# Performance work log

Measured on AMD Instinct MI355X. Metric: run time of the kernel, lower is better.

## Reference

```python
import jax, jax.numpy as jnp
import numpy as np

V, F, D, C = 100000, 512, 512, 128      # graph nodes, raw feat dim, internal_dim, num_classes
N1, S1, B1 = 36864, 32768, 4096         # layer-1 dstsrc / src / dst counts
S2, B2 = 3584, 512                      # layer-2 src / dst counts


def setup_inputs() -> dict:
    key = jax.random.key(0)
    ks = jax.random.split(key, 11)
    features = jax.random.normal(ks[0], (V, F), jnp.float32)
    src_nodes = jax.random.randint(ks[1], (N1,), 0, V)
    dst_idx1 = jax.random.randint(ks[2], (B1,), 0, N1)
    src_idx1 = jax.random.randint(ks[3], (S1,), 0, N1)
    # row-normalized diffusion matrix (minibatch generator produces mean-normalized adjacency)
    dif_mat1 = jax.random.uniform(ks[4], (B1, S1), jnp.float32) / S1
    dst_idx2 = jax.random.randint(ks[5], (B2,), 0, B1)
    src_idx2 = jax.random.randint(ks[6], (S2,), 0, B1)
    dif_mat2 = jax.random.uniform(ks[7], (B2, S2), jnp.float32) / S2
    # Glorot-ish weight init
    w1 = jax.random.normal(ks[8], (2 * F, D), jnp.float32) / np.float32(np.sqrt(2 * F))
    w2 = jax.random.normal(ks[9], (2 * D, D), jnp.float32) / np.float32(np.sqrt(2 * D))
    w_cls = jax.random.normal(ks[10], (D, C), jnp.float32) / np.float32(np.sqrt(D))
    return dict(features=features, src_nodes=src_nodes,
                dst_idx1=dst_idx1, src_idx1=src_idx1, dif_mat1=dif_mat1,
                dst_idx2=dst_idx2, src_idx2=src_idx2, dif_mat2=dif_mat2,
                w1=w1, w2=w2, w_cls=w_cls)


def _mean_aggregate(x, dst_idx, src_idx, dif_mat, w):
    # boolean_mask -> gather at selected indices
    agg = dif_mat @ x[src_idx]                       # [B, F_in]
    cat = jnp.concatenate([agg, x[dst_idx]], axis=1)  # [B, 2*F_in]
    return jax.nn.relu(cat @ w)                       # [B, D]


def reference(features, src_nodes, dst_idx1, src_idx1, dif_mat1,
              dst_idx2, src_idx2, dif_mat2, w1, w2, w_cls):
    x = features[src_nodes]                           # RawFeature: gather [N1, F]
    x = _mean_aggregate(x, dst_idx1, src_idx1, dif_mat1, w1)   # [B1, D]
    x = _mean_aggregate(x, dst_idx2, src_idx2, dif_mat2, w2)   # [B2, D]
    return jax.nn.softmax(x @ w_cls, axis=-1)          # classifier [B2, C]
```

## Files before the change

### kernel.cpp

```cpp
#include <hip/hip_runtime.h>

typedef unsigned short u16;
typedef unsigned int u32;
typedef __attribute__((ext_vector_type(8))) short short8;
typedef __attribute__((ext_vector_type(4))) float f32x4;
typedef __attribute__((ext_vector_type(8))) u16 ushort8v;

__device__ __forceinline__ u16 f2bf(float f) {
    union { float f; u32 u; } v; v.f = f;
    return (u16)((v.u + 0x7FFFu + ((v.u >> 16) & 1u)) >> 16);
}
__device__ __forceinline__ u32 pack2bf(float a, float b) {
    union { float f; u32 u; } x, y; x.f = a; y.f = b;
    u32 ra = x.u + 0x7FFFu + ((x.u >> 16) & 1u);
    u32 rb = y.u + 0x7FFFu + ((y.u >> 16) & 1u);
    return (ra >> 16) | (rb & 0xFFFF0000u);
}

__global__ __launch_bounds__(256) void gather_transpose_bf16(
    const float* __restrict__ src, const int* __restrict__ lvl1,
    const int* __restrict__ lvl2, u16* __restrict__ outT, int S)
{
    __shared__ u16 tile[32][514];
    const int s0 = blockIdx.x * 32;
    const int tid = threadIdx.x;
    const int r = tid >> 3;
    const int fb = (tid & 7) * 4;

    int row = lvl1[s0 + r];
    if (lvl2) row = lvl2[row];
    const float* sp = src + (size_t)row * 512;
    #pragma unroll
    for (int j = 0; j < 16; ++j) {
        float4 v = *(const float4*)(sp + fb + j * 32);
        *(u32*)&tile[r][fb + j * 32]     = pack2bf(v.x, v.y);
        *(u32*)&tile[r][fb + j * 32 + 2] = pack2bf(v.z, v.w);
    }
    __syncthreads();

    #pragma unroll
    for (int i = 0; i < 8; ++i) {
        int f = i * 64 + (tid >> 2);
        int sb = (tid & 3) * 8;
        ushort8v o;
        #pragma unroll
        for (int j = 0; j < 8; ++j) o[j] = tile[sb + j][f];
        *(ushort8v*)(outT + (size_t)f * S + s0 + sb) = o;
    }
}

__global__ __launch_bounds__(128) void gather_rows_f32(
    const float* __restrict__ src, const int* __restrict__ lvl1,
    const int* __restrict__ lvl2, float* __restrict__ out)
{
    int b = blockIdx.x;
    int row = lvl1[b];
    if (lvl2) row = lvl2[row];
    float4 v = *(const float4*)(src + (size_t)row * 512 + threadIdx.x * 4);
    *(float4*)(out + (size_t)b * 512 + threadIdx.x * 4) = v;
}

__global__ __launch_bounds__(256) void transpose_to_bf16(
    const float* __restrict__ in, u16* __restrict__ out, int R, int C)
{
    __shared__ float t[32][33];
    const int r0 = blockIdx.x * 32, c0 = blockIdx.y * 32;
    const int tr = threadIdx.x >> 3;
    const int tc = (threadIdx.x & 7) * 4;
    float4 v = *(const float4*)(in + (size_t)(r0 + tr) * C + c0 + tc);
    t[tr][tc] = v.x; t[tr][tc + 1] = v.y; t[tr][tc + 2] = v.z; t[tr][tc + 3] = v.w;
    __syncthreads();
    ushort4 o;
    o.x = f2bf(t[tc + 0][tr]); o.y = f2bf(t[tc + 1][tr]);
    o.z = f2bf(t[tc + 2][tr]); o.w = f2bf(t[tc + 3][tr]);
    *(ushort4*)(out + (size_t)(c0 + tr) * R + r0 + tc) = o;
}

__global__ __launch_bounds__(256, 3) void mfma_gemm_splitk(
    const float* __restrict__ A0, const float* __restrict__ A1, int K0,
    const u16* __restrict__ BT, float* __restrict__ part,
    int M, int N, int K)
{
    __shared__ u16 As[128][40];
    __shared__ u16 Bs[128][40];

    const int tid = threadIdx.x;
    const int n0 = blockIdx.x * 128;
    const int m0 = blockIdx.y * 128;
    const int kchunk = K / gridDim.z;
    const int kbeg = blockIdx.z * kchunk;
    const int kend = kbeg + kchunk;

    const int wave = tid >> 6, lane = tid & 63;
    const int wm = (wave >> 1) * 64;
    const int wn = (wave & 1) * 64;
    const int fm = lane & 15, q = lane >> 4;

    f32x4 acc[4][4];
    #pragma unroll
    for (int i = 0; i < 4; ++i)
        #pragma unroll
        for (int j = 0; j < 4; ++j) acc[i][j] = (f32x4){0.f, 0.f, 0.f, 0.f};

    const int ar = tid >> 1;
    const int ac = (tid & 1) << 4;
    const int sA1 = K - K0;

    for (int k0 = kbeg; k0 < kend; k0 += 32) {
        const float* ap = (k0 < K0)
            ? (A0 + (size_t)(m0 + ar) * K0 + k0 + ac)
            : (A1 + (size_t)(m0 + ar) * sA1 + (k0 - K0) + ac);
        float4 v0 = *(const float4*)(ap + 0);
        float4 v1 = *(const float4*)(ap + 4);
        float4 v2 = *(const float4*)(ap + 8);
        float4 v3 = *(const float4*)(ap + 12);
        uint4 w0, w1;
        w0.x = pack2bf(v0.x, v0.y); w0.y = pack2bf(v0.z, v0.w);
        w0.z = pack2bf(v1.x, v1.y); w0.w = pack2bf(v1.z, v1.w);
        w1.x = pack2bf(v2.x, v2.y); w1.y = pack2bf(v2.z, v2.w);
        w1.z = pack2bf(v3.x, v3.y); w1.w = pack2bf(v3.z, v3.w);

        const u16* bp = BT + (size_t)(n0 + ar) * K + k0 + ac;
        uint4 b0 = *(const uint4*)bp;
        uint4 b1 = *(const uint4*)(bp + 8);

        *(uint4*)&As[ar][ac]     = w0;
        *(uint4*)&As[ar][ac + 8] = w1;
        *(uint4*)&Bs[ar][ac]     = b0;
        *(uint4*)&Bs[ar][ac + 8] = b1;

        __syncthreads();

        short8 af[4], bf[4];
        #pragma unroll
        for (int mi = 0; mi < 4; ++mi)
            af[mi] = *(short8*)&As[wm + mi * 16 + fm][q * 8];
        #pragma unroll
        for (int ni = 0; ni < 4; ++ni)
            bf[ni] = *(short8*)&Bs[wn + ni * 16 + fm][q * 8];
        #pragma unroll
        for (int mi = 0; mi < 4; ++mi)
            #pragma unroll
            for (int ni = 0; ni < 4; ++ni)
                acc[mi][ni] = __builtin_amdgcn_mfma_f32_16x16x32_bf16(
                    af[mi], bf[ni], acc[mi][ni], 0, 0, 0);

        __syncthreads();
    }

    float* dst = part + (size_t)blockIdx.z * M * N;
    #pragma unroll
    for (int mi = 0; mi < 4; ++mi)
        #pragma unroll
        for (int ni = 0; ni < 4; ++ni)
            #pragma unroll
            for (int r = 0; r < 4; ++r) {
                int row = m0 + wm + mi * 16 + q * 4 + r;
                int col = n0 + wn + ni * 16 + fm;
                dst[(size_t)row * N + col] = acc[mi][ni][r];
            }
}

template<int RELU>
__global__ __launch_bounds__(256) void reduce_partials(
    const float4* __restrict__ part, float4* __restrict__ out, int MN4, int S)
{
    int i = blockIdx.x * 256 + threadIdx.x;
    if (i >= MN4) return;
    float4 a = part[i];
    for (int s = 1; s < S; ++s) {
        float4 b = part[(size_t)s * MN4 + i];
        a.x += b.x; a.y += b.y; a.z += b.z; a.w += b.w;
    }
    if (RELU) {
        a.x = fmaxf(a.x, 0.f); a.y = fmaxf(a.y, 0.f);
        a.z = fmaxf(a.z, 0.f); a.w = fmaxf(a.w, 0.f);
    }
    out[i] = a;
}

__global__ __launch_bounds__(128) void cls_softmax(
    const float* __restrict__ h2, const float* __restrict__ wcls,
    float* __restrict__ out)
{
    __shared__ float row[512];
    __shared__ float red[128];
    const int m = blockIdx.x, c = threadIdx.x;
    *(float4*)&row[c * 4] = *(const float4*)(h2 + (size_t)m * 512 + c * 4);
    __syncthreads();
    float acc = 0.f;
    #pragma unroll 8
    for (int k = 0; k < 512; ++k) acc += row[k] * wcls[k * 128 + c];
    red[c] = acc; __syncthreads();
    for (int s = 64; s > 0; s >>= 1) {
        if (c < s) red[c] = fmaxf(red[c], red[c + s]);
        __syncthreads();
    }
    float mx = red[0]; __syncthreads();
    float e = expf(acc - mx);
    red[c] = e; __syncthreads();
    for (int s = 64; s > 0; s >>= 1) {
        if (c < s) red[c] += red[c + s];
        __syncthreads();
    }
    out[(size_t)m * 128 + c] = e / red[0];
}

extern "C" void kernel_launch(void* const* d_in, const int* in_sizes, int n_in,
                              void* d_out, int out_size, void* d_ws, size_t ws_size,
                              hipStream_t stream)
{
    (void)in_sizes; (void)n_in; (void)out_size;
    const float* features  = (const float*)d_in[0];
    const int*   src_nodes = (const int*)d_in[1];
    const int*   dst_idx1  = (const int*)d_in[2];
    const int*   src_idx1  = (const int*)d_in[3];
    const float* dif1      = (const float*)d_in[4];
    const int*   dst_idx2  = (const int*)d_in[5];
    const int*   src_idx2  = (const int*)d_in[6];
    const float* dif2      = (const float*)d_in[7];
    const float* w1        = (const float*)d_in[8];
    const float* w2        = (const float*)d_in[9];
    const float* wcls      = (const float*)d_in[10];
    float* out = (float*)d_out;

    const size_t MB = 1024ull * 1024ull;
    int splits1 = (ws_size >= 102 * MB) ? 8 : ((ws_size >= 70 * MB) ? 4 : 2);

    char* ws = (char*)d_ws;
    u16*   xs1T   = (u16*)ws;
    float* agg1   = (float*)ws;
    float* xd1    = (float*)(ws + 8 * MB);
    float* h1     = (float*)(ws + 16 * MB);
    u16*   h1selT = (u16*)(ws + 24 * MB);
    float* h1dst  = (float*)(ws + 28 * MB);
    float* part   = (float*)(ws + 32 * MB);
    size_t po = 32 * MB + (size_t)splits1 * 8 * MB;
    u16*   w1T  = (u16*)(ws + po); po += MB;
    u16*   w2T  = (u16*)(ws + po); po += MB;
    float* agg2 = (float*)(ws + po); po += MB;
    float* h2   = (float*)(ws + po); po += MB;

    transpose_to_bf16<<<dim3(32, 16), 256, 0, stream>>>(w1, w1T, 1024, 512);
    transpose_to_bf16<<<dim3(32, 16), 256, 0, stream>>>(w2, w2T, 1024, 512);

    gather_transpose_bf16<<<32768 / 32, 256, 0, stream>>>(features, src_idx1, src_nodes, xs1T, 32768);

    mfma_gemm_splitk<<<dim3(4, 32, splits1), 256, 0, stream>>>(
        dif1, nullptr, 32768, xs1T, part, 4096, 512, 32768);
    reduce_partials<0><<<2048, 256, 0, stream>>>((const float4*)part, (float4*)agg1, 524288, splits1);

    gather_rows_f32<<<4096, 128, 0, stream>>>(features, dst_idx1, src_nodes, xd1);

    mfma_gemm_splitk<<<dim3(4, 32, 2), 256, 0, stream>>>(
        agg1, xd1, 512, w1T, part, 4096, 512, 1024);
    reduce_partials<1><<<2048, 256, 0, stream>>>((const float4*)part, (float4*)h1, 524288, 2);

    gather_transpose_bf16<<<3584 / 32, 256, 0, stream>>>(h1, src_idx2, nullptr, h1selT, 3584);
    gather_rows_f32<<<512, 128, 0, stream>>>(h1, dst_idx2, nullptr, h1dst);

    mfma_gemm_splitk<<<dim3(4, 4, 8), 256, 0, stream>>>(
        dif2, nullptr, 3584, h1selT, part, 512, 512, 3584);
    reduce_partials<0><<<256, 256, 0, stream>>>((const float4*)part, (float4*)agg2, 65536, 8);

    mfma_gemm_splitk<<<dim3(4, 4, 4), 256, 0, stream>>>(
        agg2, h1dst, 512, w2T, part, 512, 512, 1024);
    reduce_partials<1><<<256, 256, 0, stream>>>((const float4*)part, (float4*)h2, 65536, 4);

    cls_softmax<<<512, 128, 0, stream>>>(h2, wcls, out);
}
```

Measured before the change: 1.203 ms.

## Double-buffer LDS in split-K GEMM with XOR swizzle, XCD remap, more splits

The split-K MFMA GEMM now double-buffers its LDS tiles. The next tile's global loads are issued before the MFMAs on the current buffer, which removes one barrier per iteration. The padded LDS layout is replaced by an XOR swizzle to avoid bank conflicts, and workgroup IDs are remapped so neighbouring tiles land on the same XCD for L2 locality. The layer-2 GEMMs use more K splits, which raises occupancy but adds more partial-sum traffic to reduce.

```diff
diff --git a/kernel.cpp b/kernel.cpp
--- a/kernel.cpp
+++ b/kernel.cpp
@@ -81,20 +81,40 @@
     const u16* __restrict__ BT, float* __restrict__ part,
     int M, int N, int K)
 {
-    __shared__ u16 As[128][40];
-    __shared__ u16 Bs[128][40];
+    __shared__ u16 As[2][128][32];
+    __shared__ u16 Bs[2][128][32];
+
+    const int nwx = gridDim.x, nwy = gridDim.y;
+    const int nwg = nwx * nwy * gridDim.z;
+    const int orig = blockIdx.x + nwx * (blockIdx.y + nwy * blockIdx.z);
+    const int qq = nwg >> 3, rr = nwg & 7;
+    const int xcd = orig & 7;
+    const int wgid = (xcd < rr ? xcd * (qq + 1) : rr * (qq + 1) + (xcd - rr) * qq)
+                     + (orig >> 3);
+    const int bx = wgid % nwx;
+    const int tmp = wgid / nwx;
+    const int by = tmp % nwy;
+    const int bz = tmp / nwy;
 
     const int tid = threadIdx.x;
-    const int n0 = blockIdx.x * 128;
-    const int m0 = blockIdx.y * 128;
+    const int n0 = bx * 128;
+    const int m0 = by * 128;
     const int kchunk = K / gridDim.z;
-    const int kbeg = blockIdx.z * kchunk;
+    const int kbeg = bz * kchunk;
     const int kend = kbeg + kchunk;
 
     const int wave = tid >> 6, lane = tid & 63;
     const int wm = (wave >> 1) * 64;
     const int wn = (wave & 1) * 64;
     const int fm = lane & 15, q = lane >> 4;
+    const int fsw = (q ^ (fm & 3)) << 3;
+
+    const int ar = tid >> 1;
+    const int ac = (tid & 1) << 4;
+    const int sl0 = (tid & 1) << 1;
+    const int ps0 = ((sl0 ^ (ar & 3)) << 3);
+    const int ps1 = (((sl0 + 1) ^ (ar & 3)) << 3);
+    const int sA1 = K - K0;
 
     f32x4 acc[4][4];
     #pragma unroll
@@ -102,53 +122,69 @@
         #pragma unroll
         for (int j = 0; j < 4; ++j) acc[i][j] = (f32x4){0.f, 0.f, 0.f, 0.f};
 
-    const int ar = tid >> 1;
-    const int ac = (tid & 1) << 4;
-    const int sA1 = K - K0;
-
-    for (int k0 = kbeg; k0 < kend; k0 += 32) {
-        const float* ap = (k0 < K0)
-            ? (A0 + (size_t)(m0 + ar) * K0 + k0 + ac)
-            : (A1 + (size_t)(m0 + ar) * sA1 + (k0 - K0) + ac);
-        float4 v0 = *(const float4*)(ap + 0);
-        float4 v1 = *(const float4*)(ap + 4);
-        float4 v2 = *(const float4*)(ap + 8);
-        float4 v3 = *(const float4*)(ap + 12);
-        uint4 w0, w1;
-        w0.x = pack2bf(v0.x, v0.y); w0.y = pack2bf(v0.z, v0.w);
-        w0.z = pack2bf(v1.x, v1.y); w0.w = pack2bf(v1.z, v1.w);
-        w1.x = pack2bf(v2.x, v2.y); w1.y = pack2bf(v2.z, v2.w);
-        w1.z = pack2bf(v3.x, v3.y); w1.w = pack2bf(v3.z, v3.w);
-
-        const u16* bp = BT + (size_t)(n0 + ar) * K + k0 + ac;
-        uint4 b0 = *(const uint4*)bp;
-        uint4 b1 = *(const uint4*)(bp + 8);
-
-        *(uint4*)&As[ar][ac]     = w0;
-        *(uint4*)&As[ar][ac + 8] = w1;
-        *(uint4*)&Bs[ar][ac]     = b0;
-        *(uint4*)&Bs[ar][ac + 8] = b1;
-
+    float4 v0, v1, v2, v3;
+    uint4 b0, b1;
+
+#define LOAD_TILE(k0_) do {                                                   \
+    const float* ap = ((k0_) < K0)                                            \
+        ? (A0 + (size_t)(m0 + ar) * K0 + (k0_) + ac)                          \
+        : (A1 + (size_t)(m0 + ar) * sA1 + ((k0_) - K0) + ac);                 \
+    v0 = *(const float4*)(ap);                                                \
+    v1 = *(const float4*)(ap + 4);                                            \
+    v2 = *(const float4*)(ap + 8);                                            \
+    v3 = *(const float4*)(ap + 12);                                           \
+    const u16* bp = BT + (size_t)(n0 + ar) * K + (k0_) + ac;                  \
+    b0 = *(const uint4*)bp;                                                   \
+    b1 = *(const uint4*)(bp + 8);                                             \
+} while (0)
+
+#define WRITE_TILE(buf_) do {                                                 \
+    uint4 w0, w1;                                                             \
+    w0.x = pack2bf(v0.x, v0.y); w0.y = pack2bf(v0.z, v0.w);                   \
+    w0.z = pack2bf(v1.x, v1.y); w0.w = pack2bf(v1.z, v1.w);                   \
+    w1.x = pack2bf(v2.x, v2.y); w1.y = pack2bf(v2.z, v2.w);                   \
+    w1.z = pack2bf(v3.x, v3.y); w1.w = pack2bf(v3.z, v3.w);                   \
+    *(uint4*)&As[buf_][ar][ps0] = w0;                                         \
+    *(uint4*)&As[buf_][ar][ps1] = w1;                                         \
+    *(uint4*)&Bs[buf_][ar][ps0] = b0;                                         \
+    *(uint4*)&Bs[buf_][ar][ps1] = b1;                                         \
+} while (0)
+
+#define COMPUTE(buf_) do {                                                    \
+    short8 af[4], bfr[4];                                                     \
+    _Pragma("unroll")                                                         \
+    for (int mi = 0; mi < 4; ++mi)                                            \
+        af[mi] = *(short8*)&As[buf_][wm + mi * 16 + fm][fsw];                 \
+    _Pragma("unroll")                                                         \
+    for (int ni = 0; ni < 4; ++ni)                                            \
+        bfr[ni] = *(short8*)&Bs[buf_][wn + ni * 16 + fm][fsw];                \
+    _Pragma("unroll")                                                         \
+    for (int mi = 0; mi < 4; ++mi)                                            \
+        _Pragma("unroll")                                                     \
+        for (int ni = 0; ni < 4; ++ni)                                        \
+            acc[mi][ni] = __builtin_amdgcn_mfma_f32_16x16x32_bf16(            \
+                af[mi], bfr[ni], acc[mi][ni], 0, 0, 0);                       \
+} while (0)
+
+    LOAD_TILE(kbeg);
+    WRITE_TILE(0);
+    __syncthreads();
+
+    int cur = 0;
+    for (int k0 = kbeg + 32; k0 < kend; k0 += 32) {
+        LOAD_TILE(k0);
+        COMPUTE(cur);
+        WRITE_TILE(cur ^ 1);
         __syncthreads();
-
-        short8 af[4], bf[4];
-        #pragma unroll
-        for (int mi = 0; mi < 4; ++mi)
-            af[mi] = *(short8*)&As[wm + mi * 16 + fm][q * 8];
-        #pragma unroll
-        for (int ni = 0; ni < 4; ++ni)
-            bf[ni] = *(short8*)&Bs[wn + ni * 16 + fm][q * 8];
-        #pragma unroll
-        for (int mi = 0; mi < 4; ++mi)
-            #pragma unroll
-            for (int ni = 0; ni < 4; ++ni)
-                acc[mi][ni] = __builtin_amdgcn_mfma_f32_16x16x32_bf16(
-                    af[mi], bf[ni], acc[mi][ni], 0, 0, 0);
-
-        __syncthreads();
-    }
-
-    float* dst = part + (size_t)blockIdx.z * M * N;
+        cur ^= 1;
+    }
+    COMPUTE(cur);
+
+#undef LOAD_TILE
+#undef WRITE_TILE
+#undef COMPUTE
+
+    float* dst = part + (size_t)bz * M * N;
     #pragma unroll
     for (int mi = 0; mi < 4; ++mi)
         #pragma unroll
@@ -226,6 +262,7 @@
 
     const size_t MB = 1024ull * 1024ull;
     int splits1 = (ws_size >= 102 * MB) ? 8 : ((ws_size >= 70 * MB) ? 4 : 2);
+    int splits2 = (splits1 >= 4) ? 4 : 2;
 
     char* ws = (char*)d_ws;
     u16*   xs1T   = (u16*)ws;
@@ -252,20 +289,20 @@
 
     gather_rows_f32<<<4096, 128, 0, stream>>>(features, dst_idx1, src_nodes, xd1);
 
-    mfma_gemm_splitk<<<dim3(4, 32, 2), 256, 0, stream>>>(
+    mfma_gemm_splitk<<<dim3(4, 32, splits2), 256, 0, stream>>>(
         agg1, xd1, 512, w1T, part, 4096, 512, 1024);
-    reduce_partials<1><<<2048, 256, 0, stream>>>((const float4*)part, (float4*)h1, 524288, 2);
+    reduce_partials<1><<<2048, 256, 0, stream>>>((const float4*)part, (float4*)h1, 524288, splits2);
 
     gather_transpose_bf16<<<3584 / 32, 256, 0, stream>>>(h1, src_idx2, nullptr, h1selT, 3584);
     gather_rows_f32<<<512, 128, 0, stream>>>(h1, dst_idx2, nullptr, h1dst);
 
-    mfma_gemm_splitk<<<dim3(4, 4, 8), 256, 0, stream>>>(
+    mfma_gemm_splitk<<<dim3(4, 4, 16), 256, 0, stream>>>(
         dif2, nullptr, 3584, h1selT, part, 512, 512, 3584);
-    reduce_partials<0><<<256, 256, 0, stream>>>((const float4*)part, (float4*)agg2, 65536, 8);
-
-    mfma_gemm_splitk<<<dim3(4, 4, 4), 256, 0, stream>>>(
+    reduce_partials<0><<<256, 256, 0, stream>>>((const float4*)part, (float4*)agg2, 65536, 16);
+
+    mfma_gemm_splitk<<<dim3(4, 4, 16), 256, 0, stream>>>(
         agg2, h1dst, 512, w2T, part, 512, 512, 1024);
-    reduce_partials<1><<<256, 256, 0, stream>>>((const float4*)part, (float4*)h2, 65536, 4);
+    reduce_partials<1><<<256, 256, 0, stream>>>((const float4*)part, (float4*)h2, 65536, 16);
 
     cls_softmax<<<512, 128, 0, stream>>>(h2, wcls, out);
 }
```

Result: faster. 1.089 ms (-9.5%).
